# Kernel optimization log

Measured on AMD Instinct MI355X. Metric: run time of the kernel, lower is better.

Reference implementation:

```python
import jax, jax.numpy as jnp
import numpy as np

K = 7          # kernel_size (window)
PAD = (K - 1) // 2  # SAME padding for stride 1


def setup_inputs() -> dict:
    key = jax.random.key(0)
    ks = jax.random.split(key, 7)
    B, H, W, C, F = 8, 128, 128, 256, 256
    rs = F // 2  # rel_size
    return {
        "x": jax.random.normal(ks[0], (B, H, W, C), jnp.float32),
        "Wq": jax.random.normal(ks[1], (C, F), jnp.float32) * 0.05,
        "Wk": jax.random.normal(ks[2], (C, F), jnp.float32) * 0.05,
        "Wv": jax.random.normal(ks[3], (C, F), jnp.float32) * 0.05,
        "rel_x": jax.random.normal(ks[4], (rs, K), jnp.float32) * 0.05,
        "rel_y": jax.random.normal(ks[5], (F - rs, K), jnp.float32) * 0.05,
        "bias": jax.random.normal(ks[6], (1, 1, 1, F), jnp.float32) * (1.0 / np.sqrt(F).astype(np.float32)),
    }


def reference(x, Wq, Wk, Wv, rel_x, rel_y, bias):
    B, H, W, C = x.shape
    rs = rel_x.shape[0]
    # 1x1 conv projections (single group)
    q = jnp.einsum('bhwc,cf->bhwf', x, Wq)
    k = jnp.einsum('bhwc,cf->bhwf', x, Wk)
    v = jnp.einsum('bhwc,cf->bhwf', x, Wv)
    kp = jnp.pad(k, ((0, 0), (PAD, PAD), (PAD, PAD), (0, 0)))
    vp = jnp.pad(v, ((0, 0), (PAD, PAD), (PAD, PAD), (0, 0)))
    # window scores: sum_c q * shifted(k) -> [b,h,w,kh,kw]; avoids im2col blowup
    scores = jnp.stack([
        jnp.stack([jnp.einsum('bhwf,bhwf->bhw', q, kp[:, i:i + H, j:j + W, :])
                   for j in range(K)], axis=-1)
        for i in range(K)], axis=-2)
    # relative position terms: x-half broadcasts along rows (kh), y-half along cols (kw)
    qx = jnp.einsum('bhwx,xk->bhwk', q[..., :rs], rel_x)
    qy = jnp.einsum('bhwy,yk->bhwk', q[..., rs:], rel_y)
    scores = scores + qx[:, :, :, None, :] + qy[:, :, :, :, None]
    attn = jax.nn.softmax(scores.reshape(B, H, W, K * K), axis=-1).reshape(B, H, W, K, K)
    # attention-weighted sum over the window for each channel
    out = sum(attn[:, :, :, i, j][..., None] * vp[:, i:i + H, j:j + W, :]
              for i in range(K) for j in range(K))
    return out + bias
```

## Files before the change

### kernel.cpp

```cpp
#include <hip/hip_runtime.h>
#include <hip/hip_fp16.h>
#include <stdint.h>

typedef _Float16 half8 __attribute__((ext_vector_type(8)));
typedef _Float16 half2v __attribute__((ext_vector_type(2)));
typedef __attribute__((ext_vector_type(4))) float f32x4;

__device__ __forceinline__ unsigned short f2h(float f) {
  __half h = __float2half(f);
  unsigned short u; __builtin_memcpy(&u, &h, 2); return u;
}
__device__ __forceinline__ unsigned pk2h(float a, float b) {
  auto v = __builtin_amdgcn_cvt_pkrtz(a, b);
  unsigned u; __builtin_memcpy(&u, &v, 4); return u;
}
__device__ __forceinline__ half2v h2cast(unsigned u) {
  half2v v; __builtin_memcpy(&v, &u, 4); return v;
}

#if __has_builtin(__builtin_amdgcn_fdot2)
__device__ __forceinline__ float dot2(half2v a, half2v b, float c) {
  return __builtin_amdgcn_fdot2(a, b, c, false);
}
#else
__device__ __forceinline__ float dot2(half2v a, half2v b, float c) {
  return c + (float)a[0] * (float)b[0] + (float)a[1] * (float)b[1];
}
#endif

__device__ __forceinline__ void gl_lds16(const void* g, void* l) {
  __builtin_amdgcn_global_load_lds(
      (const __attribute__((address_space(1))) void*)g,
      (__attribute__((address_space(3))) void*)l, 16, 0, 0);
}

__global__ __launch_bounds__(256) void xcvt(const float* __restrict__ x,
                                            unsigned short* __restrict__ xh) {
  const size_t i = ((size_t)blockIdx.x * 256 + threadIdx.x) * 8;
  float4 a = *(const float4*)&x[i];
  float4 b = *(const float4*)&x[i + 4];
  uint4 o;
  o.x = pk2h(a.x, a.y); o.y = pk2h(a.z, a.w);
  o.z = pk2h(b.x, b.y); o.w = pk2h(b.z, b.w);
  *(uint4*)&xh[i] = o;
}

__global__ __launch_bounds__(256) void wconv(const float* __restrict__ Wq,
                                             const float* __restrict__ Wk,
                                             const float* __restrict__ Wv,
                                             unsigned short* __restrict__ Wb) {
  const int e = blockIdx.x;
  const int w = e >> 8;
  const int n = e & 255;
  const float* W = (w == 0) ? Wq : ((w == 1) ? Wk : Wv);
  const int k = threadIdx.x;
  Wb[(size_t)e * 256 + k] = f2h(W[(size_t)k * 256 + n]);
}

__global__ __launch_bounds__(256) void qkv_gemm(const unsigned short* __restrict__ xh,
                                                const unsigned short* __restrict__ Wb,
                                                unsigned short* __restrict__ qkv) {
  __shared__ unsigned char ldsb[32768];

  const int tid = threadIdx.x;
  const int l = tid & 63, l15 = l & 15, l4 = l >> 4;
  const int wv = tid >> 6, wr = wv >> 1, wc = wv & 1;

  const int pid = blockIdx.x;
  const int cid = (pid & 7) * 768 + (pid >> 3);
  const int by = cid / 6;
  const int bx = cid - by * 6;
  const size_t row0 = (size_t)by * 128;
  const int n0 = bx * 128;

  const int rbase0 = wv * 32, rbase1 = wv * 32 + 16;
  const int rA0 = rbase0 + (l >> 2), rA1 = rbase1 + (l >> 2);
  const int q0 = (l & 3) ^ ((rA0 >> 1) & 3), q1 = (l & 3) ^ ((rA1 >> 1) & 3);
  const unsigned short* gA0 = xh + (row0 + rA0) * 256 + q0 * 8;
  const unsigned short* gA1 = xh + (row0 + rA1) * 256 + q1 * 8;
  const unsigned short* gB0 = Wb + (size_t)(n0 + rA0) * 256 + q0 * 8;
  const unsigned short* gB1 = Wb + (size_t)(n0 + rA1) * 256 + q1 * 8;

  f32x4 acc[4][4] = {};

  auto stage = [&](int s, int d) {
    gl_lds16(gA0 + s * 32, &ldsb[d * 8192 + rbase0 * 64]);
    gl_lds16(gA1 + s * 32, &ldsb[d * 8192 + rbase1 * 64]);
    gl_lds16(gB0 + s * 32, &ldsb[16384 + d * 8192 + rbase0 * 64]);
    gl_lds16(gB1 + s * 32, &ldsb[16384 + d * 8192 + rbase1 * 64]);
  };

  stage(0, 0);
  __syncthreads();

  for (int s = 0; s < 8; ++s) {
    const int d = s & 1;
    if (s < 7) stage(s + 1, d ^ 1);
    half8 af[4], bf[4];
#pragma unroll
    for (int m = 0; m < 4; ++m) {
      const int r = wr * 64 + m * 16 + l15;
      af[m] = *(const half8*)&ldsb[d * 8192 + r * 64 + ((l4 ^ ((r >> 1) & 3)) * 16)];
    }
#pragma unroll
    for (int n = 0; n < 4; ++n) {
      const int r = wc * 64 + n * 16 + l15;
      bf[n] = *(const half8*)&ldsb[16384 + d * 8192 + r * 64 + ((l4 ^ ((r >> 1) & 3)) * 16)];
    }
#pragma unroll
    for (int n = 0; n < 4; ++n)
#pragma unroll
      for (int m = 0; m < 4; ++m)
        acc[m][n] = __builtin_amdgcn_mfma_f32_16x16x32_f16(af[m], bf[n], acc[m][n], 0, 0, 0);
    __syncthreads();
  }

#pragma unroll
  for (int m = 0; m < 4; ++m)
#pragma unroll
    for (int n = 0; n < 4; ++n) {
      const int ng = n0 + wc * 64 + n * 16 + l15;
      unsigned short* op = qkv + (size_t)(ng >> 8) * 33554432 + (ng & 255);
#pragma unroll
      for (int r = 0; r < 4; ++r) {
        const size_t grow = row0 + wr * 64 + m * 16 + l4 * 4 + r;
        op[grow * 256] = f2h(acc[m][n][r]);
      }
    }
}

__global__ __launch_bounds__(256) void qrel(const unsigned short* __restrict__ q,
                                            const float* __restrict__ relx,
                                            const float* __restrict__ rely,
                                            unsigned short* __restrict__ qr) {
  __shared__ unsigned wpk[896];
  for (int i = threadIdx.x; i < 896; i += 256) {
    const int hf = (i >= 448) ? 1 : 0;
    const int r = i - hf * 448;
    const int c2 = r / 7, j = r - c2 * 7;
    const float* R = hf ? rely : relx;
    wpk[i] = pk2h(R[(2 * c2) * 7 + j], R[(2 * c2 + 1) * 7 + j]);
  }
  __syncthreads();
  const size_t pix = (size_t)blockIdx.x * 256 + threadIdx.x;
  const uint4* qp = (const uint4*)(q + pix * 256);
  float ax[7] = {0, 0, 0, 0, 0, 0, 0}, ay[7] = {0, 0, 0, 0, 0, 0, 0};
#pragma unroll
  for (int g = 0; g < 32; ++g) {
    const uint4 u = qp[g];
    const int c2b = (g & 15) * 4;
    if (g < 16) {
#pragma unroll
      for (int j = 0; j < 7; ++j) {
        float s = ax[j];
        s = dot2(h2cast(u.x), h2cast(wpk[(c2b + 0) * 7 + j]), s);
        s = dot2(h2cast(u.y), h2cast(wpk[(c2b + 1) * 7 + j]), s);
        s = dot2(h2cast(u.z), h2cast(wpk[(c2b + 2) * 7 + j]), s);
        s = dot2(h2cast(u.w), h2cast(wpk[(c2b + 3) * 7 + j]), s);
        ax[j] = s;
      }
    } else {
#pragma unroll
      for (int j = 0; j < 7; ++j) {
        float s = ay[j];
        s = dot2(h2cast(u.x), h2cast(wpk[448 + (c2b + 0) * 7 + j]), s);
        s = dot2(h2cast(u.y), h2cast(wpk[448 + (c2b + 1) * 7 + j]), s);
        s = dot2(h2cast(u.z), h2cast(wpk[448 + (c2b + 2) * 7 + j]), s);
        s = dot2(h2cast(u.w), h2cast(wpk[448 + (c2b + 3) * 7 + j]), s);
        ay[j] = s;
      }
    }
  }
  uint4 o0, o1;
  o0.x = pk2h(ax[0], ax[1]); o0.y = pk2h(ax[2], ax[3]);
  o0.z = pk2h(ax[4], ax[5]); o0.w = pk2h(ax[6], ay[0]);
  o1.x = pk2h(ay[1], ay[2]); o1.y = pk2h(ay[3], ay[4]);
  o1.z = pk2h(ay[5], ay[6]); o1.w = 0;
  uint4* dst = (uint4*)(qr + pix * 512);
  dst[0] = o0; dst[1] = o1;
}

__global__ __launch_bounds__(256) void attn(const unsigned short* __restrict__ qkv,
                                            const float* __restrict__ bias,
                                            const unsigned short* __restrict__ qrelb,
                                            float* __restrict__ out) {
  __shared__ unsigned short kv[2][4][6688];

  const int tid = threadIdx.x;
  const int tc = tid & 31, tr = tid >> 5;

  const int pid = blockIdx.x;
  const int cid = (pid & 7) * 32 + (pid >> 3);
  const int b = cid >> 5;
  const int t5 = cid & 31;
  const int ht = t5 >> 2, wt = t5 & 3;

  const int rA = ht * 16 + 2 * tr;
  const int w = wt * 32 + tc;
  const size_t pixA = (size_t)((b * 128 + rA) * 128 + w);
  const size_t pixB = pixA + 128;

  const unsigned short* qb = qkv;
  const unsigned short* kb = qkv + 33554432;
  const unsigned short* vb = qkv + 67108864;

  long long go[4];
  bool ok[4];
#pragma unroll
  for (int k = 0; k < 4; ++k) {
    const int p = tid + k * 256;
    const int pr = p / 38, pc = p - pr * 38;
    const int gh = ht * 16 + pr - 3, gw = wt * 32 + pc - 3;
    ok[k] = (p < 836) && ((unsigned)gh < 128u) && ((unsigned)gw < 128u);
    go[k] = ((long long)((b * 128 + gh) * 128 + gw)) * 256;
  }
  const int wb8 = (tid >> 6) * 512;

  auto stage = [&](const unsigned short* base, int c, int d) {
#pragma unroll
    for (int g = 0; g < 4; ++g) {
#pragma unroll
      for (int k = 0; k < 4; ++k) {
        if (ok[k]) gl_lds16(base + go[k] + c * 32 + g * 8, &kv[d][g][k * 2048 + wb8]);
      }
    }
  };

  {
    const uint4 z = make_uint4(0u, 0u, 0u, 0u);
    for (int p = tid; p < 836; p += 256) {
      const int pr = p / 38, pc = p - pr * 38;
      const int gh = ht * 16 + pr - 3, gw = wt * 32 + pc - 3;
      if (!((unsigned)gh < 128u && (unsigned)gw < 128u)) {
#pragma unroll
        for (int d = 0; d < 2; ++d)
#pragma unroll
          for (int g = 0; g < 4; ++g)
            *(uint4*)&kv[d][g][p * 8] = z;
      }
    }
  }

  stage(kb, 0, 0);
  __syncthreads();

  float scA[49], scB[49];
#pragma unroll
  for (int t = 0; t < 49; ++t) { scA[t] = 0.0f; scB[t] = 0.0f; }

  for (int s = 0; s < 8; ++s) {
    const int d = s & 1;
    stage(s < 7 ? kb : vb, s < 7 ? s + 1 : 0, d ^ 1);
    const uint4* qAp = (const uint4*)(qb + pixA * 256 + s * 32);
    const uint4* qBp = (const uint4*)(qb + pixB * 256 + s * 32);
    uint4 a0 = qAp[0], a1 = qAp[1], a2 = qAp[2], a3 = qAp[3];
    uint4 b0 = qBp[0], b1 = qBp[1], b2 = qBp[2], b3 = qBp[3];
    half2v qhA[16], qhB[16];
    qhA[0] = h2cast(a0.x); qhA[1] = h2cast(a0.y); qhA[2] = h2cast(a0.z); qhA[3] = h2cast(a0.w);
    qhA[4] = h2cast(a1.x); qhA[5] = h2cast(a1.y); qhA[6] = h2cast(a1.z); qhA[7] = h2cast(a1.w);
    qhA[8] = h2cast(a2.x); qhA[9] = h2cast(a2.y); qhA[10] = h2cast(a2.z); qhA[11] = h2cast(a2.w);
    qhA[12] = h2cast(a3.x); qhA[13] = h2cast(a3.y); qhA[14] = h2cast(a3.z); qhA[15] = h2cast(a3.w);
    qhB[0] = h2cast(b0.x); qhB[1] = h2cast(b0.y); qhB[2] = h2cast(b0.z); qhB[3] = h2cast(b0.w);
    qhB[4] = h2cast(b1.x); qhB[5] = h2cast(b1.y); qhB[6] = h2cast(b1.z); qhB[7] = h2cast(b1.w);
    qhB[8] = h2cast(b2.x); qhB[9] = h2cast(b2.y); qhB[10] = h2cast(b2.z); qhB[11] = h2cast(b2.w);
    qhB[12] = h2cast(b3.x); qhB[13] = h2cast(b3.y); qhB[14] = h2cast(b3.z); qhB[15] = h2cast(b3.w);
    __builtin_amdgcn_s_setprio(1);
#pragma unroll
    for (int u = 0; u < 8; ++u) {
#pragma unroll
      for (int g = 0; g < 4; ++g) {
        uint4 kk[7];
#pragma unroll
        for (int j = 0; j < 7; ++j)
          kk[j] = *(const uint4*)&kv[d][g][((2 * tr + u) * 38 + tc + j) * 8];
#pragma unroll
        for (int j = 0; j < 7; ++j) {
          if (u < 7) {
            float s2 = scA[u * 7 + j];
            s2 = dot2(h2cast(kk[j].x), qhA[g * 4 + 0], s2);
            s2 = dot2(h2cast(kk[j].y), qhA[g * 4 + 1], s2);
            s2 = dot2(h2cast(kk[j].z), qhA[g * 4 + 2], s2);
            s2 = dot2(h2cast(kk[j].w), qhA[g * 4 + 3], s2);
            scA[u * 7 + j] = s2;
          }
          if (u >= 1) {
            float s2 = scB[(u - 1) * 7 + j];
            s2 = dot2(h2cast(kk[j].x), qhB[g * 4 + 0], s2);
            s2 = dot2(h2cast(kk[j].y), qhB[g * 4 + 1], s2);
            s2 = dot2(h2cast(kk[j].z), qhB[g * 4 + 2], s2);
            s2 = dot2(h2cast(kk[j].w), qhB[g * 4 + 3], s2);
            scB[(u - 1) * 7 + j] = s2;
          }
        }
      }
    }
    __builtin_amdgcn_s_setprio(0);
    __syncthreads();
  }

  {
    const uint4* rp = (const uint4*)(qrelb + pixA * 512);
    uint4 r0 = rp[0], r1 = rp[1];
    half2v c0 = h2cast(r0.x), c1 = h2cast(r0.y), c2 = h2cast(r0.z), c3 = h2cast(r0.w);
    half2v c4 = h2cast(r1.x), c5 = h2cast(r1.y), c6 = h2cast(r1.z);
    float qx[7] = {c0[0], c0[1], c1[0], c1[1], c2[0], c2[1], c3[0]};
    float qy[7] = {c3[1], c4[0], c4[1], c5[0], c5[1], c6[0], c6[1]};
#pragma unroll
    for (int i = 0; i < 7; ++i)
#pragma unroll
      for (int j = 0; j < 7; ++j) scA[i * 7 + j] += qx[j] + qy[i];
  }
  {
    const uint4* rp = (const uint4*)(qrelb + pixB * 512);
    uint4 r0 = rp[0], r1 = rp[1];
    half2v c0 = h2cast(r0.x), c1 = h2cast(r0.y), c2 = h2cast(r0.z), c3 = h2cast(r0.w);
    half2v c4 = h2cast(r1.x), c5 = h2cast(r1.y), c6 = h2cast(r1.z);
    float qx[7] = {c0[0], c0[1], c1[0], c1[1], c2[0], c2[1], c3[0]};
    float qy[7] = {c3[1], c4[0], c4[1], c5[0], c5[1], c6[0], c6[1]};
#pragma unroll
    for (int i = 0; i < 7; ++i)
#pragma unroll
      for (int j = 0; j < 7; ++j) scB[i * 7 + j] += qx[j] + qy[i];
  }

  unsigned pwp[49];
  {
    float mxA = scA[0], mxB = scB[0];
#pragma unroll
    for (int t = 1; t < 49; ++t) { mxA = fmaxf(mxA, scA[t]); mxB = fmaxf(mxB, scB[t]); }
    float sA = 0.0f, sB = 0.0f;
#pragma unroll
    for (int t = 0; t < 49; ++t) {
      float eA = __expf(scA[t] - mxA); scA[t] = eA; sA += eA;
      float eB = __expf(scB[t] - mxB); scB[t] = eB; sB += eB;
    }
    const float iA = 1.0f / sA, iB = 1.0f / sB;
#pragma unroll
    for (int t = 0; t < 49; ++t)
      pwp[t] = (unsigned)f2h(scA[t] * iA) | ((unsigned)f2h(scB[t] * iB) << 16);
  }

  for (int s = 0; s < 8; ++s) {
    const int d = s & 1;
    const int f0 = s * 32;
    if (s < 7) stage(vb, s + 1, d ^ 1);
    half2v accA[16], accB[16];
#pragma unroll
    for (int a = 0; a < 16; ++a) {
      accA[a] = half2v{(_Float16)0, (_Float16)0};
      accB[a] = half2v{(_Float16)0, (_Float16)0};
    }
    __builtin_amdgcn_s_setprio(1);
#pragma unroll
    for (int u = 0; u < 8; ++u) {
#pragma unroll
      for (int g = 0; g < 4; ++g) {
        uint4 kk[7];
#pragma unroll
        for (int j = 0; j < 7; ++j)
          kk[j] = *(const uint4*)&kv[d][g][((2 * tr + u) * 38 + tc + j) * 8];
#pragma unroll
        for (int j = 0; j < 7; ++j) {
          if (u < 7) {
            unsigned pa = pwp[u * 7 + j] & 0xffffu; pa |= pa << 16;
            const half2v p2 = h2cast(pa);
            accA[g * 4 + 0] += p2 * h2cast(kk[j].x);
            accA[g * 4 + 1] += p2 * h2cast(kk[j].y);
            accA[g * 4 + 2] += p2 * h2cast(kk[j].z);
            accA[g * 4 + 3] += p2 * h2cast(kk[j].w);
          }
          if (u >= 1) {
            unsigned pbv = pwp[(u - 1) * 7 + j] >> 16; pbv |= pbv << 16;
            const half2v p2 = h2cast(pbv);
            accB[g * 4 + 0] += p2 * h2cast(kk[j].x);
            accB[g * 4 + 1] += p2 * h2cast(kk[j].y);
            accB[g * 4 + 2] += p2 * h2cast(kk[j].z);
            accB[g * 4 + 3] += p2 * h2cast(kk[j].w);
          }
        }
      }
    }
    __builtin_amdgcn_s_setprio(0);
#pragma unroll
    for (int fq = 0; fq < 8; ++fq) {
      float4 bv = *(const float4*)&bias[f0 + fq * 4];
      float4 oA, oB;
      oA.x = (float)accA[fq * 2 + 0][0] + bv.x;
      oA.y = (float)accA[fq * 2 + 0][1] + bv.y;
      oA.z = (float)accA[fq * 2 + 1][0] + bv.z;
      oA.w = (float)accA[fq * 2 + 1][1] + bv.w;
      oB.x = (float)accB[fq * 2 + 0][0] + bv.x;
      oB.y = (float)accB[fq * 2 + 0][1] + bv.y;
      oB.z = (float)accB[fq * 2 + 1][0] + bv.z;
      oB.w = (float)accB[fq * 2 + 1][1] + bv.w;
      *(float4*)&out[pixA * 256 + f0 + fq * 4] = oA;
      *(float4*)&out[pixB * 256 + f0 + fq * 4] = oB;
    }
    if (s < 7) __syncthreads();
  }
}

extern "C" void kernel_launch(void* const* d_in, const int* in_sizes, int n_in,
                              void* d_out, int out_size, void* d_ws, size_t ws_size,
                              hipStream_t stream) {
  const float* x = (const float*)d_in[0];
  const float* Wq = (const float*)d_in[1];
  const float* Wk = (const float*)d_in[2];
  const float* Wv = (const float*)d_in[3];
  const float* relx = (const float*)d_in[4];
  const float* rely = (const float*)d_in[5];
  const float* bias = (const float*)d_in[6];
  float* out = (float*)d_out;

  unsigned short* xh = (unsigned short*)d_out;
  unsigned short* qrl = (unsigned short*)d_out;
  unsigned short* Wb = (unsigned short*)d_ws;
  unsigned short* qkv = (unsigned short*)((char*)d_ws + 393216);

  xcvt<<<dim3(16384), dim3(256), 0, stream>>>(x, xh);
  wconv<<<dim3(768), dim3(256), 0, stream>>>(Wq, Wk, Wv, Wb);
  qkv_gemm<<<dim3(6144), dim3(256), 0, stream>>>(xh, Wb, qkv);
  qrel<<<dim3(512), dim3(256), 0, stream>>>(qkv, relx, rely, qrl);
  attn<<<dim3(256), dim3(256), 0, stream>>>(qkv, bias, qrl, out);
}
```

Before: 301.1 us.

## Shrink attention tiles to 16x16 and split score channels across lane halves

The attention kernel now uses 16x16 pixel tiles instead of 32x16, doubling the grid to 512 blocks and shrinking the shared-memory K/V buffer, so more blocks can be resident per CU. In the score phase, the two 32-lane halves of each wave each take half of every 32-channel slice, and the partial scores are combined with a cross-half shuffle. In the weighted-sum phase, each half handles alternate groups of channel slices, which leaves half the lanes idle at any moment. Smaller tiles also raise the share of halo pixels loaded per tile.

```diff
diff --git a/kernel.cpp b/kernel.cpp
--- a/kernel.cpp
+++ b/kernel.cpp
@@ -184,53 +184,56 @@
                                             const float* __restrict__ bias,
                                             const unsigned short* __restrict__ qrelb,
                                             float* __restrict__ out) {
-  __shared__ unsigned short kv[2][4][6688];
+  __shared__ unsigned short kv[2][4][3872];
 
   const int tid = threadIdx.x;
-  const int tc = tid & 31, tr = tid >> 5;
+  const int wave = tid >> 6, lane = tid & 63;
+  const int half = lane >> 5;
+  const int pi = lane & 31;
+  const int pr = wave * 2 + (pi >> 4);
+  const int pcol = pi & 15;
 
   const int pid = blockIdx.x;
-  const int cid = (pid & 7) * 32 + (pid >> 3);
-  const int b = cid >> 5;
-  const int t5 = cid & 31;
-  const int ht = t5 >> 2, wt = t5 & 3;
-
-  const int rA = ht * 16 + 2 * tr;
-  const int w = wt * 32 + tc;
-  const size_t pixA = (size_t)((b * 128 + rA) * 128 + w);
+  const int cid = (pid & 7) * 64 + (pid >> 3);
+  const int b = cid >> 6;
+  const int t6 = cid & 63;
+  const int ht = t6 >> 3, wt = t6 & 7;
+
+  const int hA = ht * 16 + 2 * pr;
+  const int w = wt * 16 + pcol;
+  const size_t pixA = (size_t)((b * 128 + hA) * 128 + w);
   const size_t pixB = pixA + 128;
 
   const unsigned short* qb = qkv;
   const unsigned short* kb = qkv + 33554432;
   const unsigned short* vb = qkv + 67108864;
 
-  long long go[4];
-  bool ok[4];
-#pragma unroll
-  for (int k = 0; k < 4; ++k) {
-    const int p = tid + k * 256;
-    const int pr = p / 38, pc = p - pr * 38;
-    const int gh = ht * 16 + pr - 3, gw = wt * 32 + pc - 3;
-    ok[k] = (p < 836) && ((unsigned)gh < 128u) && ((unsigned)gw < 128u);
-    go[k] = ((long long)((b * 128 + gh) * 128 + gw)) * 256;
-  }
-  const int wb8 = (tid >> 6) * 512;
+  const int pr0 = tid / 22, pc0 = tid - pr0 * 22;
+  const int gh0 = ht * 16 + pr0 - 3, gw0 = wt * 16 + pc0 - 3;
+  const bool ok0 = ((unsigned)gh0 < 128u) && ((unsigned)gw0 < 128u);
+  const long long go0 = ((long long)((b * 128 + gh0) * 128 + gw0)) * 256;
+
+  const int p1 = tid + 256;
+  const int pr1 = p1 / 22, pc1 = p1 - pr1 * 22;
+  const int gh1 = ht * 16 + pr1 - 3, gw1 = wt * 16 + pc1 - 3;
+  const bool ok1 = (p1 < 484) && ((unsigned)gh1 < 128u) && ((unsigned)gw1 < 128u);
+  const long long go1 = ((long long)((b * 128 + gh1) * 128 + gw1)) * 256;
+
+  const int wb8 = wave * 512;
 
   auto stage = [&](const unsigned short* base, int c, int d) {
 #pragma unroll
     for (int g = 0; g < 4; ++g) {
-#pragma unroll
-      for (int k = 0; k < 4; ++k) {
-        if (ok[k]) gl_lds16(base + go[k] + c * 32 + g * 8, &kv[d][g][k * 2048 + wb8]);
-      }
+      if (ok0) gl_lds16(base + go0 + c * 32 + g * 8, &kv[d][g][wb8]);
+      if (ok1) gl_lds16(base + go1 + c * 32 + g * 8, &kv[d][g][2048 + wb8]);
     }
   };
 
   {
     const uint4 z = make_uint4(0u, 0u, 0u, 0u);
-    for (int p = tid; p < 836; p += 256) {
-      const int pr = p / 38, pc = p - pr * 38;
-      const int gh = ht * 16 + pr - 3, gw = wt * 32 + pc - 3;
+    for (int p = tid; p < 484; p += 256) {
+      const int prh = p / 22, pch = p - prh * 22;
+      const int gh = ht * 16 + prh - 3, gw = wt * 16 + pch - 3;
       if (!((unsigned)gh < 128u && (unsigned)gw < 128u)) {
 #pragma unroll
         for (int d = 0; d < 2; ++d)
@@ -251,44 +254,41 @@
   for (int s = 0; s < 8; ++s) {
     const int d = s & 1;
     stage(s < 7 ? kb : vb, s < 7 ? s + 1 : 0, d ^ 1);
-    const uint4* qAp = (const uint4*)(qb + pixA * 256 + s * 32);
-    const uint4* qBp = (const uint4*)(qb + pixB * 256 + s * 32);
-    uint4 a0 = qAp[0], a1 = qAp[1], a2 = qAp[2], a3 = qAp[3];
-    uint4 b0 = qBp[0], b1 = qBp[1], b2 = qBp[2], b3 = qBp[3];
-    half2v qhA[16], qhB[16];
+    const uint4* qAp = (const uint4*)(qb + pixA * 256 + s * 32 + half * 16);
+    const uint4* qBp = (const uint4*)(qb + pixB * 256 + s * 32 + half * 16);
+    uint4 a0 = qAp[0], a1 = qAp[1];
+    uint4 b0 = qBp[0], b1 = qBp[1];
+    half2v qhA[8], qhB[8];
     qhA[0] = h2cast(a0.x); qhA[1] = h2cast(a0.y); qhA[2] = h2cast(a0.z); qhA[3] = h2cast(a0.w);
     qhA[4] = h2cast(a1.x); qhA[5] = h2cast(a1.y); qhA[6] = h2cast(a1.z); qhA[7] = h2cast(a1.w);
-    qhA[8] = h2cast(a2.x); qhA[9] = h2cast(a2.y); qhA[10] = h2cast(a2.z); qhA[11] = h2cast(a2.w);
-    qhA[12] = h2cast(a3.x); qhA[13] = h2cast(a3.y); qhA[14] = h2cast(a3.z); qhA[15] = h2cast(a3.w);
     qhB[0] = h2cast(b0.x); qhB[1] = h2cast(b0.y); qhB[2] = h2cast(b0.z); qhB[3] = h2cast(b0.w);
     qhB[4] = h2cast(b1.x); qhB[5] = h2cast(b1.y); qhB[6] = h2cast(b1.z); qhB[7] = h2cast(b1.w);
-    qhB[8] = h2cast(b2.x); qhB[9] = h2cast(b2.y); qhB[10] = h2cast(b2.z); qhB[11] = h2cast(b2.w);
-    qhB[12] = h2cast(b3.x); qhB[13] = h2cast(b3.y); qhB[14] = h2cast(b3.z); qhB[15] = h2cast(b3.w);
     __builtin_amdgcn_s_setprio(1);
 #pragma unroll
     for (int u = 0; u < 8; ++u) {
 #pragma unroll
-      for (int g = 0; g < 4; ++g) {
+      for (int e = 0; e < 2; ++e) {
+        const int g = half * 2 + e;
         uint4 kk[7];
 #pragma unroll
         for (int j = 0; j < 7; ++j)
-          kk[j] = *(const uint4*)&kv[d][g][((2 * tr + u) * 38 + tc + j) * 8];
+          kk[j] = *(const uint4*)&kv[d][g][((2 * pr + u) * 22 + pcol + j) * 8];
 #pragma unroll
         for (int j = 0; j < 7; ++j) {
           if (u < 7) {
             float s2 = scA[u * 7 + j];
-            s2 = dot2(h2cast(kk[j].x), qhA[g * 4 + 0], s2);
-            s2 = dot2(h2cast(kk[j].y), qhA[g * 4 + 1], s2);
-            s2 = dot2(h2cast(kk[j].z), qhA[g * 4 + 2], s2);
-            s2 = dot2(h2cast(kk[j].w), qhA[g * 4 + 3], s2);
+            s2 = dot2(h2cast(kk[j].x), qhA[e * 4 + 0], s2);
+            s2 = dot2(h2cast(kk[j].y), qhA[e * 4 + 1], s2);
+            s2 = dot2(h2cast(kk[j].z), qhA[e * 4 + 2], s2);
+            s2 = dot2(h2cast(kk[j].w), qhA[e * 4 + 3], s2);
             scA[u * 7 + j] = s2;
           }
           if (u >= 1) {
             float s2 = scB[(u - 1) * 7 + j];
-            s2 = dot2(h2cast(kk[j].x), qhB[g * 4 + 0], s2);
-            s2 = dot2(h2cast(kk[j].y), qhB[g * 4 + 1], s2);
-            s2 = dot2(h2cast(kk[j].z), qhB[g * 4 + 2], s2);
-            s2 = dot2(h2cast(kk[j].w), qhB[g * 4 + 3], s2);
+            s2 = dot2(h2cast(kk[j].x), qhB[e * 4 + 0], s2);
+            s2 = dot2(h2cast(kk[j].y), qhB[e * 4 + 1], s2);
+            s2 = dot2(h2cast(kk[j].z), qhB[e * 4 + 2], s2);
+            s2 = dot2(h2cast(kk[j].w), qhB[e * 4 + 3], s2);
             scB[(u - 1) * 7 + j] = s2;
           }
         }
@@ -296,6 +296,12 @@
     }
     __builtin_amdgcn_s_setprio(0);
     __syncthreads();
+  }
+
+#pragma unroll
+  for (int t = 0; t < 49; ++t) {
+    scA[t] += __shfl_xor(scA[t], 32, 64);
+    scB[t] += __shfl_xor(scB[t], 32, 64);
   }
 
   {
@@ -344,57 +350,59 @@
     const int d = s & 1;
     const int f0 = s * 32;
     if (s < 7) stage(vb, s + 1, d ^ 1);
-    half2v accA[16], accB[16];
-#pragma unroll
-    for (int a = 0; a < 16; ++a) {
-      accA[a] = half2v{(_Float16)0, (_Float16)0};
-      accB[a] = half2v{(_Float16)0, (_Float16)0};
-    }
-    __builtin_amdgcn_s_setprio(1);
-#pragma unroll
-    for (int u = 0; u < 8; ++u) {
-#pragma unroll
-      for (int g = 0; g < 4; ++g) {
-        uint4 kk[7];
-#pragma unroll
-        for (int j = 0; j < 7; ++j)
-          kk[j] = *(const uint4*)&kv[d][g][((2 * tr + u) * 38 + tc + j) * 8];
-#pragma unroll
-        for (int j = 0; j < 7; ++j) {
-          if (u < 7) {
-            unsigned pa = pwp[u * 7 + j] & 0xffffu; pa |= pa << 16;
-            const half2v p2 = h2cast(pa);
-            accA[g * 4 + 0] += p2 * h2cast(kk[j].x);
-            accA[g * 4 + 1] += p2 * h2cast(kk[j].y);
-            accA[g * 4 + 2] += p2 * h2cast(kk[j].z);
-            accA[g * 4 + 3] += p2 * h2cast(kk[j].w);
-          }
-          if (u >= 1) {
-            unsigned pbv = pwp[(u - 1) * 7 + j] >> 16; pbv |= pbv << 16;
-            const half2v p2 = h2cast(pbv);
-            accB[g * 4 + 0] += p2 * h2cast(kk[j].x);
-            accB[g * 4 + 1] += p2 * h2cast(kk[j].y);
-            accB[g * 4 + 2] += p2 * h2cast(kk[j].z);
-            accB[g * 4 + 3] += p2 * h2cast(kk[j].w);
+    if (half == (s >> 2)) {
+      half2v accA[16], accB[16];
+#pragma unroll
+      for (int a = 0; a < 16; ++a) {
+        accA[a] = half2v{(_Float16)0, (_Float16)0};
+        accB[a] = half2v{(_Float16)0, (_Float16)0};
+      }
+      __builtin_amdgcn_s_setprio(1);
+#pragma unroll
+      for (int u = 0; u < 8; ++u) {
+#pragma unroll
+        for (int g = 0; g < 4; ++g) {
+          uint4 kk[7];
+#pragma unroll
+          for (int j = 0; j < 7; ++j)
+            kk[j] = *(const uint4*)&kv[d][g][((2 * pr + u) * 22 + pcol + j) * 8];
+#pragma unroll
+          for (int j = 0; j < 7; ++j) {
+            if (u < 7) {
+              unsigned pa = pwp[u * 7 + j] & 0xffffu; pa |= pa << 16;
+              const half2v p2 = h2cast(pa);
+              accA[g * 4 + 0] += p2 * h2cast(kk[j].x);
+              accA[g * 4 + 1] += p2 * h2cast(kk[j].y);
+              accA[g * 4 + 2] += p2 * h2cast(kk[j].z);
+              accA[g * 4 + 3] += p2 * h2cast(kk[j].w);
+            }
+            if (u >= 1) {
+              unsigned pbv = pwp[(u - 1) * 7 + j] >> 16; pbv |= pbv << 16;
+              const half2v p2 = h2cast(pbv);
+              accB[g * 4 + 0] += p2 * h2cast(kk[j].x);
+              accB[g * 4 + 1] += p2 * h2cast(kk[j].y);
+              accB[g * 4 + 2] += p2 * h2cast(kk[j].z);
+              accB[g * 4 + 3] += p2 * h2cast(kk[j].w);
+            }
           }
         }
       }
-    }
-    __builtin_amdgcn_s_setprio(0);
-#pragma unroll
-    for (int fq = 0; fq < 8; ++fq) {
-      float4 bv = *(const float4*)&bias[f0 + fq * 4];
-      float4 oA, oB;
-      oA.x = (float)accA[fq * 2 + 0][0] + bv.x;
-      oA.y = (float)accA[fq * 2 + 0][1] + bv.y;
-      oA.z = (float)accA[fq * 2 + 1][0] + bv.z;
-      oA.w = (float)accA[fq * 2 + 1][1] + bv.w;
-      oB.x = (float)accB[fq * 2 + 0][0] + bv.x;
-      oB.y = (float)accB[fq * 2 + 0][1] + bv.y;
-      oB.z = (float)accB[fq * 2 + 1][0] + bv.z;
-      oB.w = (float)accB[fq * 2 + 1][1] + bv.w;
-      *(float4*)&out[pixA * 256 + f0 + fq * 4] = oA;
-      *(float4*)&out[pixB * 256 + f0 + fq * 4] = oB;
+      __builtin_amdgcn_s_setprio(0);
+#pragma unroll
+      for (int fq = 0; fq < 8; ++fq) {
+        float4 bv = *(const float4*)&bias[f0 + fq * 4];
+        float4 oA, oB;
+        oA.x = (float)accA[fq * 2 + 0][0] + bv.x;
+        oA.y = (float)accA[fq * 2 + 0][1] + bv.y;
+        oA.z = (float)accA[fq * 2 + 1][0] + bv.z;
+        oA.w = (float)accA[fq * 2 + 1][1] + bv.w;
+        oB.x = (float)accB[fq * 2 + 0][0] + bv.x;
+        oB.y = (float)accB[fq * 2 + 0][1] + bv.y;
+        oB.z = (float)accB[fq * 2 + 1][0] + bv.z;
+        oB.w = (float)accB[fq * 2 + 1][1] + bv.w;
+        *(float4*)&out[pixA * 256 + f0 + fq * 4] = oA;
+        *(float4*)&out[pixB * 256 + f0 + fq * 4] = oB;
+      }
     }
     if (s < 7) __syncthreads();
   }
@@ -421,5 +429,5 @@
   wconv<<<dim3(768), dim3(256), 0, stream>>>(Wq, Wk, Wv, Wb);
   qkv_gemm<<<dim3(6144), dim3(256), 0, stream>>>(xh, Wb, qkv);
   qrel<<<dim3(512), dim3(256), 0, stream>>>(qkv, relx, rely, qrl);
-  attn<<<dim3(256), dim3(256), 0, stream>>>(qkv, bias, qrl, out);
-}
+  attn<<<dim3(512), dim3(256), 0, stream>>>(qkv, bias, qrl, out);
+}
```

New measurement: 289.0 us. 1.04x faster.
